# Kernel tuning notes

Hardware: AMD Instinct MI355X
Metric: run time of the kernel (lower is better)

Reference implementation:

```python
import jax, jax.numpy as jnp
import numpy as np

UP_KERNEL = 5  # CARAFEPack default
SCALE = 2


def conv2d(x, w, b, padding=0):
    out = jax.lax.conv_general_dilated(
        x, w, window_strides=(1, 1),
        padding=[(padding, padding), (padding, padding)],
        dimension_numbers=("NCHW", "OIHW", "NCHW"))
    return out + b[None, :, None, None]


def pixel_shuffle(x, s):
    n, c, h, w = x.shape
    co = c // (s * s)
    x = x.reshape(n, co, s, s, h, w)
    x = x.transpose(0, 1, 4, 2, 5, 3)  # n, co, h, s, w, s
    return x.reshape(n, co, h * s, w * s)


def setup_inputs() -> dict:
    key = jax.random.key(0)
    ks = jax.random.split(key, 7)
    inp = {
        "x": jax.random.normal(ks[0], (8, 1, 513, 513), jnp.float32),
        "conv_w": jax.random.normal(ks[1], (1, 1, 2, 2), jnp.float32) * 0.5,
        "conv_b": jax.random.normal(ks[2], (1,), jnp.float32) * 0.1,
        "comp_w": jax.random.normal(ks[3], (64, 1, 1, 1), jnp.float32) * 0.5,
        "comp_b": jax.random.normal(ks[4], (64,), jnp.float32) * 0.1,
        "enc_w": jax.random.normal(ks[5], (100, 64, 3, 3), jnp.float32) * 0.05,
        "enc_b": jax.random.normal(ks[6], (100,), jnp.float32) * 0.1,
    }
    return inp


def reference(x, conv_w, conv_b, comp_w, comp_b, enc_w, enc_b):
    k, s = UP_KERNEL, SCALE
    # leading valid conv, kernel 2 -> [N,1,H,W] with H=W=512
    feat = conv2d(x, conv_w, conv_b, padding=0)
    n, c, h, w = feat.shape
    # CARAFEPack: compress channels, predict reassembly kernels
    comp = conv2d(feat, comp_w, comp_b, padding=0)          # [N,64,H,W]
    mask = conv2d(comp, enc_w, enc_b, padding=1)            # [N,k^2*s^2,H,W]
    mask = pixel_shuffle(mask, s)                            # [N,k^2,sH,sW]
    mask = jax.nn.softmax(mask, axis=1)                      # normalize over k^2
    # unfold feat into kxk neighborhoods (pad = (k-1)//2)
    pad = (k - 1) // 2
    xp = jnp.pad(feat, ((0, 0), (0, 0), (pad, pad), (pad, pad)))
    patches = jnp.stack(
        [xp[:, :, i:i + h, j:j + w] for i in range(k) for j in range(k)],
        axis=2)                                              # [N,C,k^2,H,W]
    # each output pixel (h*s+a, w*s+b) uses the kernel at that upsampled loc
    maskr = mask.reshape(n, k * k, h, s, w, s)
    out = jnp.einsum("nckhw,nkhawb->nchawb", patches, maskr)
    return out.reshape(n, c, h * s, w * s)
```

## Files before the change

### kernel.cpp

```cpp
#include <hip/hip_runtime.h>

typedef float v2f    __attribute__((ext_vector_type(2)));
typedef float f32x16 __attribute__((ext_vector_type(16)));
typedef __bf16 bf16x8 __attribute__((ext_vector_type(8)));

#define H 512
#define W 512
#define XH 513
#define L2E 1.4426950408889634f

#define WS_DELTA 2048

__device__ inline void row2ch(int r, int& q, int& j) {
  q = (r & 1) + 2 * ((r >> 2) & 1);
  j = ((r >> 1) & 1) + 2 * ((r >> 3) & 3) + 8 * (r >> 5);
}

__device__ inline unsigned bf16_rne(float f) {
  unsigned u = __float_as_uint(f);
  return (u + 0x7FFFu + ((u >> 16) & 1u)) >> 16;
}

__device__ inline unsigned cvtpk(float lo, float hi_) {
  unsigned r;
  asm("v_cvt_pk_bf16_f32 %0, %1, %2" : "=v"(r) : "v"(lo), "v"(hi_));
  return r;
}

__global__ __launch_bounds__(1024)
void prep_kernel(const float* comp_w, const float* comp_b,
                 const float* enc_w, const float* enc_b,
                 unsigned* ws) {
  __shared__ float sWe[900];
  __shared__ float sBc[900];
  int t = threadIdx.x;
  if (t < 900) {
    int o = t / 9, tap = t % 9;
    float sw = 0.f, sb = 0.f;
    for (int c = 0; c < 64; ++c) {
      float e = enc_w[(o * 64 + c) * 9 + tap];
      sw += e * comp_w[c];
      sb += e * comp_b[c];
    }
    sWe[t] = sw * L2E;
    sBc[t] = sb * L2E;
  }
  __syncthreads();
  if (t < 128) {
    int r = t, q, j;
    row2ch(r, q, j);
    unsigned k1[16], k2[16];
    #pragma unroll
    for (int k = 0; k < 16; ++k) { k1[k] = 0; k2[k] = 0; }
    if (j < 25) {
      int o = j * 4 + q;
      unsigned wh[9], wl[9];
      float base = enc_b[o] * L2E;
      for (int tap = 0; tap < 9; ++tap) base += sBc[o * 9 + tap];
      for (int tap = 0; tap < 9; ++tap) {
        float wf = sWe[o * 9 + tap];
        unsigned h = bf16_rne(wf);
        wh[tap] = h;
        wl[tap] = bf16_rne(wf - __uint_as_float(h << 16));
      }
      unsigned bh = bf16_rne(base);
      unsigned bl = bf16_rne(base - __uint_as_float(bh << 16));
      for (int tap = 0; tap < 9; ++tap) k1[tap] = wh[tap];
      k1[9] = bh;
      for (int tap = 0; tap < 6; ++tap) k1[10 + tap] = wh[tap];
      for (int tap = 0; tap < 3; ++tap) k2[tap] = wh[6 + tap];
      for (int tap = 0; tap < 9; ++tap) k2[3 + tap] = wl[tap];
      k2[12] = bl;
    }
    int tt = r >> 5, m = r & 31;
    for (int kh = 0; kh < 2; ++kh) {
      int lane = m + 32 * kh;
      for (int d = 0; d < 4; ++d) {
        int k = kh * 8 + d * 2;
        ws[((0 * 4 + tt) * 64 + lane) * 4 + d] = k1[k] | (k1[k + 1] << 16);
        ws[((1 * 4 + tt) * 64 + lane) * 4 + d] = k2[k] | (k2[k + 1] << 16);
      }
    }
  }
  if (t < 1024) {
    int pat = (t >> 7) + 1, r = t & 127, q, j;
    row2ch(r, q, j);
    float dv = 0.f;
    if (j < 25) {
      int o = j * 4 + q;
      int ph = pat / 3, pw_ = pat % 3;
      for (int tap = 0; tap < 9; ++tap) {
        int dr = tap / 3, dc = tap % 3;
        bool bad = (ph == 1 && dr == 0) || (ph == 2 && dr == 2) ||
                   (pw_ == 1 && dc == 0) || (pw_ == 2 && dc == 2);
        if (bad) dv -= sBc[o * 9 + tap];
      }
    }
    ((float*)ws)[WS_DELTA + t] = dv;
  }
}

__global__ __launch_bounds__(64, 4)
void carafe_kernel(const float* x, const float* conv_w, const float* conv_b,
                   const unsigned* ws, float* out) {
  __shared__ float sF[13][36];
  __shared__ float sDelta[8][128];

  int lane = threadIdx.x;
  int n = blockIdx.z;
  int w0 = blockIdx.x * 32;
  int y0 = blockIdx.y * 8;

  float w00 = conv_w[0], w01 = conv_w[1], w10 = conv_w[2], w11 = conv_w[3];
  float cb = conv_b[0];
  const float* xn = x + (size_t)n * XH * XH;

  for (int i = lane; i < 13 * 36; i += 64) {
    int r = i / 36, c = i - r * 36;
    int hh = y0 - 2 + r, ww = w0 - 2 + c;
    float v = 0.f;
    if (hh >= 0 && hh < H && ww >= 0 && ww < W) {
      const float* p = xn + (size_t)hh * XH + ww;
      v = cb + w00 * p[0] + w01 * p[1] + w10 * p[XH] + w11 * p[XH + 1];
    }
    sF[r][c] = v;
  }
  bool borderblk = (blockIdx.x == 0) | (blockIdx.x == 15) |
                   (blockIdx.y == 0) | (blockIdx.y == 63);
  if (borderblk)
    for (int i = lane; i < 1024; i += 64)
      ((float*)sDelta)[i] = ((const float*)ws)[WS_DELTA + i];

  int pc = lane & 31, hi = lane >> 5;

  int4 A1[4], A2[4];
  #pragma unroll
  for (int t = 0; t < 4; ++t) {
    A1[t] = *(const int4*)(ws + ((0 * 4 + t) * 64 + lane) * 4);
    A2[t] = *(const int4*)(ws + ((1 * 4 + t) * 64 + lane) * 4);
  }
  __syncthreads();

  int wx = w0 + pc;
  float one = 1.0f;

  float tp[3][3];
  #pragma unroll
  for (int i = 0; i < 3; ++i)
    #pragma unroll
    for (int j = 0; j < 3; ++j)
      tp[i][j] = sF[1 + i][pc + 1 + j];

  const float* frow0 = &sF[0][pc];

  const f32x16 zeroacc = {0.f};
  int pwp = (wx == 0) ? 1 : ((wx == W - 1) ? 2 : 0);

  #pragma unroll
  for (int rr = 0; rr < 8; ++rr) {
    int hpx = y0 + rr;

    float t0 = tp[0][0], t1 = tp[0][1], t2 = tp[0][2];
    float t3 = tp[1][0], t4 = tp[1][1], t5 = tp[1][2];
    float t6 = tp[2][0], t7 = tp[2][1], t8 = tp[2][2];
    unsigned d01 = cvtpk(t0, t1), d23 = cvtpk(t2, t3);
    unsigned d45 = cvtpk(t4, t5), d67 = cvtpk(t6, t7);
    unsigned d8x = cvtpk(t8, one);
    float fl0 = t0 - __uint_as_float(d01 << 16);
    float fl1 = t1 - __uint_as_float(d01 & 0xFFFF0000u);
    float fl2 = t2 - __uint_as_float(d23 << 16);
    float fl3 = t3 - __uint_as_float(d23 & 0xFFFF0000u);
    float fl4 = t4 - __uint_as_float(d45 << 16);
    float fl5 = t5 - __uint_as_float(d45 & 0xFFFF0000u);
    float fl6 = t6 - __uint_as_float(d67 << 16);
    float fl7 = t7 - __uint_as_float(d67 & 0xFFFF0000u);
    float fl8 = t8 - __uint_as_float(d8x << 16);
    unsigned l01 = cvtpk(fl0, fl1), l23 = cvtpk(fl2, fl3);
    unsigned l45 = cvtpk(fl4, fl5), l67 = cvtpk(fl6, fl7);

    int4 b1, b2;
    b1.x = hi ? d8x : d01;
    b1.y = hi ? l01 : d23;
    b1.z = hi ? l23 : d45;
    b1.w = hi ? l45 : d67;
    b2.x = hi ? cvtpk(t5, t6) : l67;
    b2.y = hi ? cvtpk(t7, t8) : cvtpk(fl8, t0);
    b2.z = hi ? 0x00003F80u : cvtpk(t1, t2);
    b2.w = hi ? 0u : cvtpk(t3, t4);

    int ph = (hpx == 0) ? 1 : ((hpx == H - 1) ? 2 : 0);
    int pat = ph * 3 + pwp;
    bool anyb = __any(pat != 0);

    v2f sP0 = {0.f, 0.f}, aP0 = {0.f, 0.f};
    v2f sP1 = {0.f, 0.f}, aP1 = {0.f, 0.f};
    #pragma unroll
    for (int t = 0; t < 4; ++t) {
      f32x16 acc = __builtin_amdgcn_mfma_f32_32x32x16_bf16(
          __builtin_bit_cast(bf16x8, A1[t]), __builtin_bit_cast(bf16x8, b1),
          zeroacc, 0, 0, 0);
      acc = __builtin_amdgcn_mfma_f32_32x32x16_bf16(
          __builtin_bit_cast(bf16x8, A2[t]), __builtin_bit_cast(bf16x8, b2),
          acc, 0, 0, 0);
      if (anyb && pat != 0) {
        const float* dl = &sDelta[pat - 1][4 * hi];
        #pragma unroll
        for (int g = 0; g < 16; ++g) {
          if (t == 3 && g > 1) continue;
          acc[g] += dl[(g & 3) + 8 * (g >> 2) + 32 * t];
        }
      }
      #pragma unroll
      for (int jl = 0; jl < 8; ++jl) {
        if (t == 3 && jl > 0) continue;
        int j = 8 * t + jl;
        v2f e;
        e.x = __builtin_amdgcn_exp2f(acc[2 * jl + 0]);
        e.y = __builtin_amdgcn_exp2f(acc[2 * jl + 1]);
        float fj = frow0[(rr + j / 5) * 36 + (j % 5)];
        if (t & 1) { sP1 += e; aP1 += e * fj; }
        else       { sP0 += e; aP0 += e * fj; }
      }
      __builtin_amdgcn_sched_barrier(0);
    }
    v2f s01 = sP0 + sP1;
    v2f a01 = aP0 + aP1;

    float2 res;
    res.x = a01.x * __builtin_amdgcn_rcpf(s01.x);
    res.y = a01.y * __builtin_amdgcn_rcpf(s01.y);
    float* prow = out + ((size_t)n * 1024 + 2 * hpx + hi) * 1024 + 2 * wx;
    *(float2*)prow = res;

    if (rr < 7) {
      #pragma unroll
      for (int i = 0; i < 2; ++i)
        #pragma unroll
        for (int j = 0; j < 3; ++j)
          tp[i][j] = tp[i + 1][j];
      #pragma unroll
      for (int j = 0; j < 3; ++j)
        tp[2][j] = sF[rr + 4][pc + 1 + j];
    }
  }
}

extern "C" void kernel_launch(void* const* d_in, const int* in_sizes, int n_in,
                              void* d_out, int out_size, void* d_ws, size_t ws_size,
                              hipStream_t stream) {
  const float* x      = (const float*)d_in[0];
  const float* conv_w = (const float*)d_in[1];
  const float* conv_b = (const float*)d_in[2];
  const float* comp_w = (const float*)d_in[3];
  const float* comp_b = (const float*)d_in[4];
  const float* enc_w  = (const float*)d_in[5];
  const float* enc_b  = (const float*)d_in[6];
  float* out = (float*)d_out;
  unsigned* ws = (unsigned*)d_ws;

  prep_kernel<<<1, 1024, 0, stream>>>(comp_w, comp_b, enc_w, enc_b, ws);
  carafe_kernel<<<dim3(16, 64, 8), 64, 0, stream>>>(x, conv_w, conv_b, ws, out);
}
```

Measured before the change: 72.13 us.

## Split CARAFE into interior and border kernels with LDS-staged weight fragments

Splits the main kernel into an interior kernel, which drops all bounds checks and border-delta corrections, and a separate border kernel that covers the outer ring of tiles. The interior kernel stages the MFMA A fragments in LDS and reloads them per MFMA step instead of holding 32 VGPRs, to cut register pressure. The border kernel keeps a 5x5 register window and removes the scheduling barrier. Costs are an extra kernel launch, a serialized border pass with low occupancy, and extra LDS reads with explicit waitcnt stalls.

```diff
diff --git a/kernel.cpp b/kernel.cpp
--- a/kernel.cpp
+++ b/kernel.cpp
@@ -101,15 +101,19 @@
 }
 
 __global__ __launch_bounds__(64, 4)
-void carafe_kernel(const float* x, const float* conv_w, const float* conv_b,
-                   const unsigned* ws, float* out) {
+void carafe_int_kernel(const float* __restrict__ x, const float* __restrict__ conv_w,
+                       const float* __restrict__ conv_b,
+                       const unsigned* __restrict__ ws, float* __restrict__ out) {
+  __shared__ __align__(16) int4 sA[512];
   __shared__ float sF[13][36];
-  __shared__ float sDelta[8][128];
 
   int lane = threadIdx.x;
   int n = blockIdx.z;
-  int w0 = blockIdx.x * 32;
-  int y0 = blockIdx.y * 8;
+  int w0 = (blockIdx.x + 1) * 32;
+  int y0 = (blockIdx.y + 1) * 8;
+
+  for (int i = lane; i < 512; i += 64)
+    sA[i] = ((const int4*)ws)[i];
 
   float w00 = conv_w[0], w01 = conv_w[1], w10 = conv_w[2], w11 = conv_w[3];
   float cb = conv_b[0];
@@ -117,29 +121,13 @@
 
   for (int i = lane; i < 13 * 36; i += 64) {
     int r = i / 36, c = i - r * 36;
-    int hh = y0 - 2 + r, ww = w0 - 2 + c;
-    float v = 0.f;
-    if (hh >= 0 && hh < H && ww >= 0 && ww < W) {
-      const float* p = xn + (size_t)hh * XH + ww;
-      v = cb + w00 * p[0] + w01 * p[1] + w10 * p[XH] + w11 * p[XH + 1];
-    }
-    sF[r][c] = v;
-  }
-  bool borderblk = (blockIdx.x == 0) | (blockIdx.x == 15) |
-                   (blockIdx.y == 0) | (blockIdx.y == 63);
-  if (borderblk)
-    for (int i = lane; i < 1024; i += 64)
-      ((float*)sDelta)[i] = ((const float*)ws)[WS_DELTA + i];
+    const float* p = xn + (size_t)(y0 - 2 + r) * XH + (w0 - 2 + c);
+    sF[r][c] = cb + w00 * p[0] + w01 * p[1] + w10 * p[XH] + w11 * p[XH + 1];
+  }
+  __syncthreads();
 
   int pc = lane & 31, hi = lane >> 5;
-
-  int4 A1[4], A2[4];
-  #pragma unroll
-  for (int t = 0; t < 4; ++t) {
-    A1[t] = *(const int4*)(ws + ((0 * 4 + t) * 64 + lane) * 4);
-    A2[t] = *(const int4*)(ws + ((1 * 4 + t) * 64 + lane) * 4);
-  }
-  __syncthreads();
+  unsigned abase = (unsigned)(size_t)(&sA[0]) + (unsigned)lane * 16u;
 
   int wx = w0 + pc;
   float one = 1.0f;
@@ -152,9 +140,7 @@
       tp[i][j] = sF[1 + i][pc + 1 + j];
 
   const float* frow0 = &sF[0][pc];
-
   const f32x16 zeroacc = {0.f};
-  int pwp = (wx == 0) ? 1 : ((wx == W - 1) ? 2 : 0);
 
   #pragma unroll
   for (int rr = 0; rr < 8; ++rr) {
@@ -188,6 +174,144 @@
     b2.z = hi ? 0x00003F80u : cvtpk(t1, t2);
     b2.w = hi ? 0u : cvtpk(t3, t4);
 
+    v2f sP0 = {0.f, 0.f}, aP0 = {0.f, 0.f};
+    v2f sP1 = {0.f, 0.f}, aP1 = {0.f, 0.f};
+    #pragma unroll
+    for (int t = 0; t < 4; ++t) {
+      unsigned at = abase + (unsigned)(t * 1024);
+      int4 a1, a2;
+      asm volatile("ds_read_b128 %0, %2\n\t"
+                   "ds_read_b128 %1, %2 offset:4096\n\t"
+                   "s_waitcnt lgkmcnt(0)"
+                   : "=v"(a1), "=v"(a2) : "v"(at));
+      f32x16 acc = __builtin_amdgcn_mfma_f32_32x32x16_bf16(
+          __builtin_bit_cast(bf16x8, a1), __builtin_bit_cast(bf16x8, b1),
+          zeroacc, 0, 0, 0);
+      acc = __builtin_amdgcn_mfma_f32_32x32x16_bf16(
+          __builtin_bit_cast(bf16x8, a2), __builtin_bit_cast(bf16x8, b2),
+          acc, 0, 0, 0);
+      #pragma unroll
+      for (int jl = 0; jl < 8; ++jl) {
+        if (t == 3 && jl > 0) continue;
+        int j = 8 * t + jl;
+        v2f e;
+        e.x = __builtin_amdgcn_exp2f(acc[2 * jl + 0]);
+        e.y = __builtin_amdgcn_exp2f(acc[2 * jl + 1]);
+        float fj = frow0[(rr + j / 5) * 36 + (j % 5)];
+        if (t & 1) { sP1 += e; aP1 += e * fj; }
+        else       { sP0 += e; aP0 += e * fj; }
+      }
+      __builtin_amdgcn_sched_barrier(0);
+    }
+    v2f s01 = sP0 + sP1;
+    v2f a01 = aP0 + aP1;
+
+    float2 res;
+    res.x = a01.x * __builtin_amdgcn_rcpf(s01.x);
+    res.y = a01.y * __builtin_amdgcn_rcpf(s01.y);
+    float* prow = out + ((size_t)n * 1024 + 2 * hpx + hi) * 1024 + 2 * wx;
+    *(float2*)prow = res;
+
+    if (rr < 7) {
+      #pragma unroll
+      for (int i = 0; i < 2; ++i)
+        #pragma unroll
+        for (int j = 0; j < 3; ++j)
+          tp[i][j] = tp[i + 1][j];
+      #pragma unroll
+      for (int j = 0; j < 3; ++j)
+        tp[2][j] = sF[rr + 4][pc + 1 + j];
+    }
+  }
+}
+
+__global__ __launch_bounds__(64, 3)
+void carafe_brd_kernel(const float* x, const float* conv_w, const float* conv_b,
+                       const unsigned* ws, float* out) {
+  __shared__ float sF[13][36];
+  __shared__ float sDelta[8][128];
+
+  int lane = threadIdx.x;
+  int n = blockIdx.z;
+  int bi = blockIdx.x;
+  int bx, by;
+  if (bi < 128) { bx = (bi & 1) ? 15 : 0; by = bi >> 1; }
+  else { int rem = bi - 128; bx = 1 + rem % 14; by = (rem / 14) ? 63 : 0; }
+  int w0 = bx * 32;
+  int y0 = by * 8;
+
+  float w00 = conv_w[0], w01 = conv_w[1], w10 = conv_w[2], w11 = conv_w[3];
+  float cb = conv_b[0];
+  const float* xn = x + (size_t)n * XH * XH;
+
+  for (int i = lane; i < 13 * 36; i += 64) {
+    int r = i / 36, c = i - r * 36;
+    int hh = y0 - 2 + r, ww = w0 - 2 + c;
+    float v = 0.f;
+    if (hh >= 0 && hh < H && ww >= 0 && ww < W) {
+      const float* p = xn + (size_t)hh * XH + ww;
+      v = cb + w00 * p[0] + w01 * p[1] + w10 * p[XH] + w11 * p[XH + 1];
+    }
+    sF[r][c] = v;
+  }
+  for (int i = lane; i < 1024; i += 64)
+    ((float*)sDelta)[i] = ((const float*)ws)[WS_DELTA + i];
+
+  int pc = lane & 31, hi = lane >> 5;
+
+  int4 A1[4], A2[4];
+  #pragma unroll
+  for (int t = 0; t < 4; ++t) {
+    A1[t] = *(const int4*)(ws + ((0 * 4 + t) * 64 + lane) * 4);
+    A2[t] = *(const int4*)(ws + ((1 * 4 + t) * 64 + lane) * 4);
+  }
+  __syncthreads();
+
+  int wx = w0 + pc;
+  float one = 1.0f;
+
+  float p[5][5];
+  #pragma unroll
+  for (int i = 0; i < 5; ++i)
+    #pragma unroll
+    for (int j = 0; j < 5; ++j)
+      p[i][j] = sF[i][pc + j];
+
+  const f32x16 zeroacc = {0.f};
+  int pwp = (wx == 0) ? 1 : ((wx == W - 1) ? 2 : 0);
+
+  #pragma unroll
+  for (int rr = 0; rr < 8; ++rr) {
+    int hpx = y0 + rr;
+
+    float t0 = p[1][1], t1 = p[1][2], t2 = p[1][3];
+    float t3 = p[2][1], t4 = p[2][2], t5 = p[2][3];
+    float t6 = p[3][1], t7 = p[3][2], t8 = p[3][3];
+    unsigned d01 = cvtpk(t0, t1), d23 = cvtpk(t2, t3);
+    unsigned d45 = cvtpk(t4, t5), d67 = cvtpk(t6, t7);
+    unsigned d8x = cvtpk(t8, one);
+    float fl0 = t0 - __uint_as_float(d01 << 16);
+    float fl1 = t1 - __uint_as_float(d01 & 0xFFFF0000u);
+    float fl2 = t2 - __uint_as_float(d23 << 16);
+    float fl3 = t3 - __uint_as_float(d23 & 0xFFFF0000u);
+    float fl4 = t4 - __uint_as_float(d45 << 16);
+    float fl5 = t5 - __uint_as_float(d45 & 0xFFFF0000u);
+    float fl6 = t6 - __uint_as_float(d67 << 16);
+    float fl7 = t7 - __uint_as_float(d67 & 0xFFFF0000u);
+    float fl8 = t8 - __uint_as_float(d8x << 16);
+    unsigned l01 = cvtpk(fl0, fl1), l23 = cvtpk(fl2, fl3);
+    unsigned l45 = cvtpk(fl4, fl5), l67 = cvtpk(fl6, fl7);
+
+    int4 b1, b2;
+    b1.x = hi ? d8x : d01;
+    b1.y = hi ? l01 : d23;
+    b1.z = hi ? l23 : d45;
+    b1.w = hi ? l45 : d67;
+    b2.x = hi ? cvtpk(t5, t6) : l67;
+    b2.y = hi ? cvtpk(t7, t8) : cvtpk(fl8, t0);
+    b2.z = hi ? 0x00003F80u : cvtpk(t1, t2);
+    b2.w = hi ? 0u : cvtpk(t3, t4);
+
     int ph = (hpx == 0) ? 1 : ((hpx == H - 1) ? 2 : 0);
     int pat = ph * 3 + pwp;
     bool anyb = __any(pat != 0);
@@ -217,11 +341,10 @@
         v2f e;
         e.x = __builtin_amdgcn_exp2f(acc[2 * jl + 0]);
         e.y = __builtin_amdgcn_exp2f(acc[2 * jl + 1]);
-        float fj = frow0[(rr + j / 5) * 36 + (j % 5)];
+        float fj = p[j / 5][j % 5];
         if (t & 1) { sP1 += e; aP1 += e * fj; }
         else       { sP0 += e; aP0 += e * fj; }
       }
-      __builtin_amdgcn_sched_barrier(0);
     }
     v2f s01 = sP0 + sP1;
     v2f a01 = aP0 + aP1;
@@ -234,13 +357,13 @@
 
     if (rr < 7) {
       #pragma unroll
-      for (int i = 0; i < 2; ++i)
+      for (int i = 0; i < 4; ++i)
         #pragma unroll
-        for (int j = 0; j < 3; ++j)
-          tp[i][j] = tp[i + 1][j];
-      #pragma unroll
-      for (int j = 0; j < 3; ++j)
-        tp[2][j] = sF[rr + 4][pc + 1 + j];
+        for (int j = 0; j < 5; ++j)
+          p[i][j] = p[i + 1][j];
+      #pragma unroll
+      for (int j = 0; j < 5; ++j)
+        p[4][j] = sF[rr + 5][pc + j];
     }
   }
 }
@@ -259,5 +382,6 @@
   unsigned* ws = (unsigned*)d_ws;
 
   prep_kernel<<<1, 1024, 0, stream>>>(comp_w, comp_b, enc_w, enc_b, ws);
-  carafe_kernel<<<dim3(16, 64, 8), 64, 0, stream>>>(x, conv_w, conv_b, ws, out);
-}
+  carafe_int_kernel<<<dim3(14, 62, 8), 64, 0, stream>>>(x, conv_w, conv_b, ws, out);
+  carafe_brd_kernel<<<dim3(156, 1, 8), 64, 0, stream>>>(x, conv_w, conv_b, ws, out);
+}
```

New measurement: 73.12 us. About the same (+1.4%).
